# Optimization experiments

Hardware: AMD Instinct MI355X
Metric: run time of the kernel (lower is better)

The kernel has to match this reference:

```python
import jax, jax.numpy as jnp
import numpy as np

EMBED_DIM = 1024
NUM_HEADS = 16
HEAD_DIM = EMBED_DIM // NUM_HEADS
EPS = 1e-5


def setup_inputs() -> dict:
    key = jax.random.key(0)
    ks = jax.random.split(key, 7)
    B, S, D = 4, 2048, EMBED_DIM
    s = 1.0 / np.sqrt(D)
    return {
        "x": jax.random.normal(ks[0], (B, S, D), dtype=jnp.float32),
        "W_qkv": jax.random.uniform(ks[1], (D, 3 * D), jnp.float32, -s, s),
        "b_qkv": jax.random.uniform(ks[2], (3 * D,), jnp.float32, -s, s),
        "W_out": jax.random.uniform(ks[3], (D, D), jnp.float32, -s, s),
        "b_out": jax.random.uniform(ks[4], (D,), jnp.float32, -s, s),
        "gamma": jnp.ones((D,), jnp.float32),
        "beta": jnp.zeros((D,), jnp.float32),
    }


def _layer_norm(y, gamma, beta):
    mu = jnp.mean(y, axis=-1, keepdims=True)
    var = jnp.mean(jnp.square(y - mu), axis=-1, keepdims=True)
    return (y - mu) * jax.lax.rsqrt(var + EPS) * gamma + beta


def reference(x, W_qkv, b_qkv, W_out, b_out, gamma, beta):
    B, S, D = x.shape
    H, Hd = NUM_HEADS, HEAD_DIM
    qkv = x @ W_qkv + b_qkv                       # [B,S,3D]
    q, k, v = jnp.split(qkv, 3, axis=-1)
    q = q.reshape(B, S, H, Hd).transpose(0, 2, 1, 3)  # [B,H,S,Hd]
    k = k.reshape(B, S, H, Hd).transpose(0, 2, 1, 3)
    v = v.reshape(B, S, H, Hd).transpose(0, 2, 1, 3)
    scale = 1.0 / np.sqrt(Hd)
    scores = jnp.einsum("bhsd,bhtd->bhst", q, k) * scale  # [B,H,S,S]
    attn = jax.nn.softmax(scores, axis=-1)
    ctx = jnp.einsum("bhst,bhtd->bhsd", attn, v)  # [B,H,S,Hd]
    ctx = ctx.transpose(0, 2, 1, 3).reshape(B, S, D)
    out = ctx @ W_out + b_out
    return _layer_norm(out + x, gamma, beta)
```

## Files before the change

### kernel.cpp

```cpp
#include <hip/hip_runtime.h>
#include <stdint.h>
#include <stddef.h>


#define SEQ    2048
#define DMODEL 1024
#define NHEAD  16
#define HDIM   64

typedef __attribute__((ext_vector_type(4))) float f32x4;
typedef __attribute__((ext_vector_type(16))) float f32x16;
typedef __attribute__((ext_vector_type(8))) short bf16x8;
typedef __attribute__((ext_vector_type(2))) unsigned uint2v;

static __device__ __forceinline__ unsigned short f2b(float f) {
  union { float f; unsigned u; } c; c.f = f;
  unsigned r = c.u + 0x7FFFu + ((c.u >> 16) & 1u);
  return (unsigned short)(r >> 16);
}
static __device__ __forceinline__ unsigned pkbf(float lo, float hi_) {
  unsigned r;
  asm("v_cvt_pk_bf16_f32 %0, %1, %2" : "=v"(r) : "v"(lo), "v"(hi_));
  return r;
}
static __device__ __forceinline__ float exp2v(float x) {
  return __builtin_amdgcn_exp2f(x);
}
static __device__ __forceinline__ uint2v swap32(unsigned a, unsigned b) {
  return __builtin_amdgcn_permlane32_swap(a, b, false, false);
}
static __device__ __forceinline__ void gl_lds16(const void* g, void* l) {
  __builtin_amdgcn_global_load_lds((const __attribute__((address_space(1))) void*)g,
                                   (__attribute__((address_space(3))) void*)l, 16, 0, 0);
}
static __device__ __forceinline__ int swz(int row, int col) {
  return (row * 64 + col) ^ ((row & 7) << 3);
}

__global__ __launch_bounds__(256) void k_cvt(const float* __restrict__ in,
                                             unsigned short* __restrict__ out) {
  const size_t i = ((size_t)blockIdx.x * 256 + threadIdx.x) * 8;
  f32x4 a = *(const f32x4*)&in[i];
  f32x4 b = *(const f32x4*)&in[i + 4];
  bf16x8 o;
  o[0] = (short)f2b(a[0]); o[1] = (short)f2b(a[1]);
  o[2] = (short)f2b(a[2]); o[3] = (short)f2b(a[3]);
  o[4] = (short)f2b(b[0]); o[5] = (short)f2b(b[1]);
  o[6] = (short)f2b(b[2]); o[7] = (short)f2b(b[3]);
  *(bf16x8*)&out[i] = o;
}

__global__ __launch_bounds__(256) void k_transpose_cvt(const float* __restrict__ in,
                                                       unsigned short* __restrict__ out,
                                                       int R, int C) {
  __shared__ unsigned short tile[32][33];
  const int c0 = blockIdx.x * 32, r0 = blockIdx.y * 32;
  const int tx = threadIdx.x, ty = threadIdx.y;
#pragma unroll
  for (int j = 0; j < 4; j++) {
    int rr = ty + j * 8;
    tile[rr][tx] = f2b(in[(size_t)(r0 + rr) * C + c0 + tx]);
  }
  __syncthreads();
#pragma unroll
  for (int j = 0; j < 4; j++) {
    int rr = ty + j * 8;
    out[(size_t)(c0 + rr) * R + r0 + tx] = tile[tx][rr];
  }
}

__global__ __launch_bounds__(256) void k_gemm_qkv(const unsigned short* __restrict__ X,
                                                  const unsigned short* __restrict__ WT,
                                                  const float* __restrict__ bias,
                                                  unsigned short* __restrict__ qb,
                                                  unsigned short* __restrict__ kb,
                                                  unsigned short* __restrict__ vt) {
  __shared__ __align__(16) unsigned short As[128 * 32];
  __shared__ __align__(16) unsigned short Bs[128 * 32];
  const int t = threadIdx.x;
  const int w = t >> 6, l = t & 63, g = l >> 4, r = l & 15;
  const int wr = w >> 1, wc = w & 1;
  const int bm = blockIdx.x * 128;
  const int bn = blockIdx.y * 128;

  f32x4 acc[4][4];
#pragma unroll
  for (int a = 0; a < 4; a++)
#pragma unroll
    for (int b = 0; b < 4; b++) acc[a][b] = f32x4{0.f, 0.f, 0.f, 0.f};

  for (int k0 = 0; k0 < DMODEL; k0 += 32) {
    __syncthreads();
#pragma unroll
    for (int j = 0; j < 2; j++) {
      int idx = t + j * 256;
      int row = idx >> 2, kc = idx & 3;
      gl_lds16(X + (size_t)(bm + row) * DMODEL + k0 + kc * 8, (char*)As + idx * 16);
      gl_lds16(WT + (size_t)(bn + row) * DMODEL + k0 + kc * 8, (char*)Bs + idx * 16);
    }
    __syncthreads();
    bf16x8 af[4], bf[4];
#pragma unroll
    for (int mf = 0; mf < 4; mf++)
      af[mf] = *(const bf16x8*)&As[(wr * 64 + mf * 16 + r) * 32 + g * 8];
#pragma unroll
    for (int nf = 0; nf < 4; nf++)
      bf[nf] = *(const bf16x8*)&Bs[(wc * 64 + nf * 16 + r) * 32 + g * 8];
#pragma unroll
    for (int mf = 0; mf < 4; mf++)
#pragma unroll
      for (int nf = 0; nf < 4; nf++)
        acc[mf][nf] = __builtin_amdgcn_mfma_f32_16x16x32_bf16(af[mf], bf[nf], acc[mf][nf], 0, 0, 0);
  }

#pragma unroll
  for (int mf = 0; mf < 4; mf++)
#pragma unroll
    for (int nf = 0; nf < 4; nf++)
#pragma unroll
      for (int i = 0; i < 4; i++) {
        int m = bm + wr * 64 + mf * 16 + g * 4 + i;
        int n = bn + wc * 64 + nf * 16 + r;
        float v = acc[mf][nf][i] + bias[n];
        int part = n >> 10, rem = n & 1023, h = rem >> 6, d = rem & 63;
        int bi = m >> 11, s = m & 2047;
        int bh = bi * NHEAD + h;
        if (part == 0)      qb[((size_t)bh * SEQ + s) * HDIM + d] = f2b(v * 0.18033688f);
        else if (part == 1) kb[((size_t)bh * SEQ + s) * HDIM + d] = f2b(v);
        else                vt[((size_t)bh * HDIM + d) * SEQ + s] = f2b(v);
      }
}

__global__ __launch_bounds__(256) void k_attn(const unsigned short* __restrict__ qb,
                                              const unsigned short* __restrict__ kb,
                                              const unsigned short* __restrict__ vt,
                                              unsigned short* __restrict__ ctx) {
  __shared__ __align__(16) unsigned short Qs[128 * 64];
  __shared__ __align__(16) unsigned short K0[64 * 64];
  __shared__ __align__(16) unsigned short V0[64 * 64];
  const int t = threadIdx.x;
  const int w = t >> 6, l = t & 63;
  const int ql = l & 31, hi = l >> 5;
  const int q0 = blockIdx.x * 128;
  const int bh = blockIdx.y;
  const size_t qoff = ((size_t)bh * SEQ + q0) * HDIM;

#pragma unroll
  for (int j = 0; j < 4; j++) {
    int idx = t + j * 256;
    int row = idx >> 3, s = idx & 7;
    gl_lds16(qb + qoff + (size_t)row * 64 + (s ^ (row & 7)) * 8, (char*)Qs + idx * 16);
  }
#pragma unroll
  for (int j = 0; j < 2; j++) {
    int idx = t + j * 256;
    int row = idx >> 3, s = idx & 7;
    gl_lds16(kb + ((size_t)bh * SEQ + row) * HDIM + (s ^ (row & 7)) * 8, (char*)K0 + idx * 16);
    gl_lds16(vt + ((size_t)bh * HDIM + row) * SEQ + (s ^ (row & 7)) * 8, (char*)V0 + idx * 16);
  }
  asm volatile("s_waitcnt vmcnt(4)" ::: "memory");
  __builtin_amdgcn_sched_barrier(0);
  __builtin_amdgcn_s_barrier();

  bf16x8 qf[4];
#pragma unroll
  for (int ds = 0; ds < 4; ds++)
    qf[ds] = *(const bf16x8*)&Qs[swz(w * 32 + ql, ds * 16 + hi * 8)];
  asm volatile("s_waitcnt lgkmcnt(0)" ::: "memory");
  __builtin_amdgcn_sched_barrier(0);
  __builtin_amdgcn_s_barrier();

  bf16x8 ones;
#pragma unroll
  for (int i = 0; i < 8; i++) ones[i] = (short)0x3F80;

  f32x16 acc_o[2];
  f32x16 acc_l;
#pragma unroll
  for (int db = 0; db < 2; db++)
#pragma unroll
    for (int i = 0; i < 16; i++) acc_o[db][i] = 0.f;
#pragma unroll
  for (int i = 0; i < 16; i++) acc_l[i] = 0.f;

  for (int it = 0; it < SEQ / 64; ++it) {
    const int b = it & 1;
    if (it + 1 < SEQ / 64) {
      const int kt = (it + 1) * 64;
      unsigned short* Kd = (b ^ 1) ? Qs : K0;
      unsigned short* Vd = (b ^ 1) ? (Qs + 4096) : V0;
#pragma unroll
      for (int j = 0; j < 2; j++) {
        int idx = t + j * 256;
        int row = idx >> 3, s = idx & 7;
        gl_lds16(kb + ((size_t)bh * SEQ + kt + row) * HDIM + (s ^ (row & 7)) * 8,
                 (char*)Kd + idx * 16);
        gl_lds16(vt + ((size_t)bh * HDIM + row) * SEQ + kt + (s ^ (row & 7)) * 8,
                 (char*)Vd + idx * 16);
      }
      asm volatile("s_waitcnt vmcnt(4)" ::: "memory");
    } else {
      asm volatile("s_waitcnt vmcnt(0)" ::: "memory");
    }
    __builtin_amdgcn_sched_barrier(0);
    __builtin_amdgcn_s_barrier();

    const unsigned short* Kb = b ? Qs : K0;
    const unsigned short* Vb = b ? (Qs + 4096) : V0;

    bf16x8 kf[2][4];
#pragma unroll
    for (int kb2 = 0; kb2 < 2; kb2++)
#pragma unroll
      for (int ds = 0; ds < 4; ds++)
        kf[kb2][ds] = *(const bf16x8*)&Kb[swz(kb2 * 32 + ql, ds * 16 + hi * 8)];

    f32x16 accs[2];
#pragma unroll
    for (int kb2 = 0; kb2 < 2; kb2++)
#pragma unroll
      for (int i = 0; i < 16; i++) accs[kb2][i] = 0.f;
    __builtin_amdgcn_s_setprio(1);
#pragma unroll
    for (int ds = 0; ds < 4; ds++)
#pragma unroll
      for (int kb2 = 0; kb2 < 2; kb2++)
        accs[kb2] = __builtin_amdgcn_mfma_f32_32x32x16_bf16(kf[kb2][ds], qf[ds], accs[kb2], 0, 0, 0);
    __builtin_amdgcn_s_setprio(0);

#pragma unroll
    for (int kb2 = 0; kb2 < 2; kb2++)
#pragma unroll
      for (int i = 0; i < 16; i++) accs[kb2][i] = exp2v(accs[kb2][i]);

    bf16x8 pa[4];
#pragma unroll
    for (int ks = 0; ks < 4; ks++) {
      const int kb2 = ks >> 1, rb = (ks & 1) * 8;
      unsigned wA0 = pkbf(accs[kb2][rb + 0], accs[kb2][rb + 1]);
      unsigned wA1 = pkbf(accs[kb2][rb + 2], accs[kb2][rb + 3]);
      unsigned wB0 = pkbf(accs[kb2][rb + 4], accs[kb2][rb + 5]);
      unsigned wB1 = pkbf(accs[kb2][rb + 6], accs[kb2][rb + 7]);
      uint2v s0 = swap32(wB0, wA0);
      uint2v s1 = swap32(wB1, wA1);
      union { bf16x8 v; unsigned u[4]; } fr;
      fr.u[0] = s0[1]; fr.u[1] = s1[1]; fr.u[2] = s0[0]; fr.u[3] = s1[0];
      pa[ks] = fr.v;
    }

    bf16x8 vf[2][4];
#pragma unroll
    for (int db = 0; db < 2; db++)
#pragma unroll
      for (int ks = 0; ks < 4; ks++)
        vf[db][ks] = *(const bf16x8*)&Vb[swz(db * 32 + ql, ks * 16 + hi * 8)];

    __builtin_amdgcn_s_setprio(1);
#pragma unroll
    for (int ks = 0; ks < 4; ks++) {
#pragma unroll
      for (int db = 0; db < 2; db++)
        acc_o[db] = __builtin_amdgcn_mfma_f32_32x32x16_bf16(vf[db][ks], pa[ks], acc_o[db], 0, 0, 0);
      acc_l = __builtin_amdgcn_mfma_f32_32x32x16_bf16(ones, pa[ks], acc_l, 0, 0, 0);
    }
    __builtin_amdgcn_s_setprio(0);

    __builtin_amdgcn_s_barrier();
  }

  const int bi = bh >> 4, h = bh & 15;
  const float rl = 1.f / acc_l[0];
  unsigned short* Ls = Qs + w * 2048;
#pragma unroll
  for (int db = 0; db < 2; db++)
#pragma unroll
    for (int j = 0; j < 8; j++) {
      const int d0 = db * 32 + (j & 1) * 2 + (j >> 1) * 8 + hi * 4;
      *(unsigned*)&Ls[(ql * 64 + d0) ^ ((ql & 7) << 3)] =
          pkbf(acc_o[db][2 * j] * rl, acc_o[db][2 * j + 1] * rl);
    }
#pragma unroll
  for (int rq = 0; rq < 4; rq++) {
    const int q = rq * 8 + (l >> 3);
    const int c8 = l & 7;
    bf16x8 ov = *(const bf16x8*)&Ls[(q * 64 + c8 * 8) ^ ((q & 7) << 3)];
    *(bf16x8*)&ctx[((size_t)bi * SEQ + q0 + w * 32 + q) * DMODEL + h * 64 + c8 * 8] = ov;
  }
}

__global__ __launch_bounds__(256) void k_gemm_out(const unsigned short* __restrict__ A,
                                                  const unsigned short* __restrict__ WT,
                                                  const float* __restrict__ bias,
                                                  const float* __restrict__ X,
                                                  float* __restrict__ Y) {
  __shared__ __align__(16) unsigned short As[128 * 32];
  __shared__ __align__(16) unsigned short Bs[128 * 32];
  const int t = threadIdx.x;
  const int w = t >> 6, l = t & 63, g = l >> 4, r = l & 15;
  const int wr = w >> 1, wc = w & 1;
  const int bm = blockIdx.x * 128;
  const int bn = blockIdx.y * 128;

  f32x4 acc[4][4];
#pragma unroll
  for (int a = 0; a < 4; a++)
#pragma unroll
    for (int b = 0; b < 4; b++) acc[a][b] = f32x4{0.f, 0.f, 0.f, 0.f};

  for (int k0 = 0; k0 < DMODEL; k0 += 32) {
    __syncthreads();
#pragma unroll
    for (int j = 0; j < 2; j++) {
      int idx = t + j * 256;
      int row = idx >> 2, kc = idx & 3;
      gl_lds16(A + (size_t)(bm + row) * DMODEL + k0 + kc * 8, (char*)As + idx * 16);
      gl_lds16(WT + (size_t)(bn + row) * DMODEL + k0 + kc * 8, (char*)Bs + idx * 16);
    }
    __syncthreads();
    bf16x8 af[4], bf[4];
#pragma unroll
    for (int mf = 0; mf < 4; mf++)
      af[mf] = *(const bf16x8*)&As[(wr * 64 + mf * 16 + r) * 32 + g * 8];
#pragma unroll
    for (int nf = 0; nf < 4; nf++)
      bf[nf] = *(const bf16x8*)&Bs[(wc * 64 + nf * 16 + r) * 32 + g * 8];
#pragma unroll
    for (int mf = 0; mf < 4; mf++)
#pragma unroll
      for (int nf = 0; nf < 4; nf++)
        acc[mf][nf] = __builtin_amdgcn_mfma_f32_16x16x32_bf16(af[mf], bf[nf], acc[mf][nf], 0, 0, 0);
  }

#pragma unroll
  for (int mf = 0; mf < 4; mf++)
#pragma unroll
    for (int nf = 0; nf < 4; nf++)
#pragma unroll
      for (int i = 0; i < 4; i++) {
        int m = bm + wr * 64 + mf * 16 + g * 4 + i;
        int n = bn + wc * 64 + nf * 16 + r;
        float v = acc[mf][nf][i] + bias[n] + X[(size_t)m * DMODEL + n];
        Y[(size_t)m * DMODEL + n] = v;
      }
}

__global__ __launch_bounds__(256) void k_ln(const float* __restrict__ Y,
                                            const float* __restrict__ gamma,
                                            const float* __restrict__ beta,
                                            float* __restrict__ out) {
  const int row = blockIdx.x, t = threadIdx.x;
  const float* y = Y + (size_t)row * DMODEL;
  f32x4 v = *(const f32x4*)&y[t * 4];
  float s = v[0] + v[1] + v[2] + v[3];
  float q = v[0] * v[0] + v[1] * v[1] + v[2] * v[2] + v[3] * v[3];
#pragma unroll
  for (int m = 1; m < 64; m <<= 1) { s += __shfl_xor(s, m); q += __shfl_xor(q, m); }
  __shared__ float ss[4], sq[4];
  const int w = t >> 6, l = t & 63;
  if (l == 0) { ss[w] = s; sq[w] = q; }
  __syncthreads();
  s = ss[0] + ss[1] + ss[2] + ss[3];
  q = sq[0] + sq[1] + sq[2] + sq[3];
  const float mu = s * (1.f / DMODEL);
  const float var = q * (1.f / DMODEL) - mu * mu;
  const float rs = rsqrtf(var + 1e-5f);
  f32x4 o;
#pragma unroll
  for (int j = 0; j < 4; j++)
    o[j] = (v[j] - mu) * rs * gamma[t * 4 + j] + beta[t * 4 + j];
  *(f32x4*)&out[(size_t)row * DMODEL + t * 4] = o;
}

extern "C" void kernel_launch(void* const* d_in, const int* in_sizes, int n_in,
                              void* d_out, int out_size, void* d_ws, size_t ws_size,
                              hipStream_t stream) {
  const float* X     = (const float*)d_in[0];
  const float* Wqkv  = (const float*)d_in[1];
  const float* bqkv  = (const float*)d_in[2];
  const float* Wout  = (const float*)d_in[3];
  const float* bout  = (const float*)d_in[4];
  const float* gamma = (const float*)d_in[5];
  const float* beta  = (const float*)d_in[6];

  char* ws = (char*)d_ws;
  unsigned short* wqkvT = (unsigned short*)(ws);
  unsigned short* woutT = (unsigned short*)(ws + 6291456);
  unsigned short* Xb    = (unsigned short*)(ws + 8388608);
  unsigned short* ctx   = (unsigned short*)(ws + 8388608);
  unsigned short* qb    = (unsigned short*)(ws + 25165824);
  unsigned short* kb    = (unsigned short*)(ws + 41943040);
  unsigned short* vt    = (unsigned short*)(ws + 58720256);
  float*          Yf    = (float*)d_out;

  dim3 tb(32, 8, 1);
  k_transpose_cvt<<<dim3(96, 32, 1), tb, 0, stream>>>(Wqkv, wqkvT, 1024, 3072);
  k_transpose_cvt<<<dim3(32, 32, 1), tb, 0, stream>>>(Wout, woutT, 1024, 1024);
  k_cvt<<<dim3(4096, 1, 1), dim3(256, 1, 1), 0, stream>>>(X, Xb);
  k_gemm_qkv<<<dim3(64, 24, 1), dim3(256, 1, 1), 0, stream>>>(Xb, wqkvT, bqkv, qb, kb, vt);
  k_attn<<<dim3(16, 64, 1), dim3(256, 1, 1), 0, stream>>>(qb, kb, vt, ctx);
  k_gemm_out<<<dim3(64, 8, 1), dim3(256, 1, 1), 0, stream>>>(ctx, woutT, bout, X, Yf);
  k_ln<<<dim3(8192, 1, 1), dim3(256, 1, 1), 0, stream>>>(Yf, gamma, beta, (float*)d_out);
}
```

Before: 232.7 us.

## Double-buffer LDS tiles and remap block IDs in QKV and output GEMMs

```diff
diff --git a/kernel.cpp b/kernel.cpp
--- a/kernel.cpp
+++ b/kernel.cpp
@@ -75,13 +75,15 @@
                                                   unsigned short* __restrict__ qb,
                                                   unsigned short* __restrict__ kb,
                                                   unsigned short* __restrict__ vt) {
-  __shared__ __align__(16) unsigned short As[128 * 32];
-  __shared__ __align__(16) unsigned short Bs[128 * 32];
+  __shared__ __align__(16) unsigned short As[2][128 * 32];
+  __shared__ __align__(16) unsigned short Bs[2][128 * 32];
   const int t = threadIdx.x;
   const int w = t >> 6, l = t & 63, g = l >> 4, r = l & 15;
   const int wr = w >> 1, wc = w & 1;
-  const int bm = blockIdx.x * 128;
-  const int bn = blockIdx.y * 128;
+  int id = blockIdx.x;
+  id = (id & 7) * 192 + (id >> 3);
+  const int bm = (id & 63) * 128;
+  const int bn = (id >> 6) * 128;
 
   f32x4 acc[4][4];
 #pragma unroll
@@ -89,28 +91,46 @@
 #pragma unroll
     for (int b = 0; b < 4; b++) acc[a][b] = f32x4{0.f, 0.f, 0.f, 0.f};
 
-  for (int k0 = 0; k0 < DMODEL; k0 += 32) {
-    __syncthreads();
-#pragma unroll
-    for (int j = 0; j < 2; j++) {
-      int idx = t + j * 256;
-      int row = idx >> 2, kc = idx & 3;
-      gl_lds16(X + (size_t)(bm + row) * DMODEL + k0 + kc * 8, (char*)As + idx * 16);
-      gl_lds16(WT + (size_t)(bn + row) * DMODEL + k0 + kc * 8, (char*)Bs + idx * 16);
-    }
-    __syncthreads();
+#pragma unroll
+  for (int j = 0; j < 2; j++) {
+    int idx = t + j * 256;
+    int row = idx >> 2, kc = idx & 3;
+    gl_lds16(X + (size_t)(bm + row) * DMODEL + kc * 8, (char*)As[0] + idx * 16);
+    gl_lds16(WT + (size_t)(bn + row) * DMODEL + kc * 8, (char*)Bs[0] + idx * 16);
+  }
+
+  for (int it = 0; it < DMODEL / 32; ++it) {
+    const int cur = it & 1;
+    if (it + 1 < DMODEL / 32) {
+      const int k0 = (it + 1) * 32;
+#pragma unroll
+      for (int j = 0; j < 2; j++) {
+        int idx = t + j * 256;
+        int row = idx >> 2, kc = idx & 3;
+        gl_lds16(X + (size_t)(bm + row) * DMODEL + k0 + kc * 8, (char*)As[cur ^ 1] + idx * 16);
+        gl_lds16(WT + (size_t)(bn + row) * DMODEL + k0 + kc * 8, (char*)Bs[cur ^ 1] + idx * 16);
+      }
+      asm volatile("s_waitcnt vmcnt(4)" ::: "memory");
+    } else {
+      asm volatile("s_waitcnt vmcnt(0)" ::: "memory");
+    }
+    __builtin_amdgcn_sched_barrier(0);
+    __builtin_amdgcn_s_barrier();
+
     bf16x8 af[4], bf[4];
 #pragma unroll
     for (int mf = 0; mf < 4; mf++)
-      af[mf] = *(const bf16x8*)&As[(wr * 64 + mf * 16 + r) * 32 + g * 8];
+      af[mf] = *(const bf16x8*)&As[cur][(wr * 64 + mf * 16 + r) * 32 + g * 8];
 #pragma unroll
     for (int nf = 0; nf < 4; nf++)
-      bf[nf] = *(const bf16x8*)&Bs[(wc * 64 + nf * 16 + r) * 32 + g * 8];
+      bf[nf] = *(const bf16x8*)&Bs[cur][(wc * 64 + nf * 16 + r) * 32 + g * 8];
 #pragma unroll
     for (int mf = 0; mf < 4; mf++)
 #pragma unroll
       for (int nf = 0; nf < 4; nf++)
         acc[mf][nf] = __builtin_amdgcn_mfma_f32_16x16x32_bf16(af[mf], bf[nf], acc[mf][nf], 0, 0, 0);
+
+    __builtin_amdgcn_s_barrier();
   }
 
 #pragma unroll
@@ -293,13 +313,15 @@
                                                   const float* __restrict__ bias,
                                                   const float* __restrict__ X,
                                                   float* __restrict__ Y) {
-  __shared__ __align__(16) unsigned short As[128 * 32];
-  __shared__ __align__(16) unsigned short Bs[128 * 32];
+  __shared__ __align__(16) unsigned short As[2][128 * 32];
+  __shared__ __align__(16) unsigned short Bs[2][128 * 32];
   const int t = threadIdx.x;
   const int w = t >> 6, l = t & 63, g = l >> 4, r = l & 15;
   const int wr = w >> 1, wc = w & 1;
-  const int bm = blockIdx.x * 128;
-  const int bn = blockIdx.y * 128;
+  int id = blockIdx.x;
+  id = (id & 7) * 64 + (id >> 3);
+  const int bm = (id & 63) * 128;
+  const int bn = (id >> 6) * 128;
 
   f32x4 acc[4][4];
 #pragma unroll
@@ -307,28 +329,46 @@
 #pragma unroll
     for (int b = 0; b < 4; b++) acc[a][b] = f32x4{0.f, 0.f, 0.f, 0.f};
 
-  for (int k0 = 0; k0 < DMODEL; k0 += 32) {
-    __syncthreads();
-#pragma unroll
-    for (int j = 0; j < 2; j++) {
-      int idx = t + j * 256;
-      int row = idx >> 2, kc = idx & 3;
-      gl_lds16(A + (size_t)(bm + row) * DMODEL + k0 + kc * 8, (char*)As + idx * 16);
-      gl_lds16(WT + (size_t)(bn + row) * DMODEL + k0 + kc * 8, (char*)Bs + idx * 16);
-    }
-    __syncthreads();
+#pragma unroll
+  for (int j = 0; j < 2; j++) {
+    int idx = t + j * 256;
+    int row = idx >> 2, kc = idx & 3;
+    gl_lds16(A + (size_t)(bm + row) * DMODEL + kc * 8, (char*)As[0] + idx * 16);
+    gl_lds16(WT + (size_t)(bn + row) * DMODEL + kc * 8, (char*)Bs[0] + idx * 16);
+  }
+
+  for (int it = 0; it < DMODEL / 32; ++it) {
+    const int cur = it & 1;
+    if (it + 1 < DMODEL / 32) {
+      const int k0 = (it + 1) * 32;
+#pragma unroll
+      for (int j = 0; j < 2; j++) {
+        int idx = t + j * 256;
+        int row = idx >> 2, kc = idx & 3;
+        gl_lds16(A + (size_t)(bm + row) * DMODEL + k0 + kc * 8, (char*)As[cur ^ 1] + idx * 16);
+        gl_lds16(WT + (size_t)(bn + row) * DMODEL + k0 + kc * 8, (char*)Bs[cur ^ 1] + idx * 16);
+      }
+      asm volatile("s_waitcnt vmcnt(4)" ::: "memory");
+    } else {
+      asm volatile("s_waitcnt vmcnt(0)" ::: "memory");
+    }
+    __builtin_amdgcn_sched_barrier(0);
+    __builtin_amdgcn_s_barrier();
+
     bf16x8 af[4], bf[4];
 #pragma unroll
     for (int mf = 0; mf < 4; mf++)
-      af[mf] = *(const bf16x8*)&As[(wr * 64 + mf * 16 + r) * 32 + g * 8];
+      af[mf] = *(const bf16x8*)&As[cur][(wr * 64 + mf * 16 + r) * 32 + g * 8];
 #pragma unroll
     for (int nf = 0; nf < 4; nf++)
-      bf[nf] = *(const bf16x8*)&Bs[(wc * 64 + nf * 16 + r) * 32 + g * 8];
+      bf[nf] = *(const bf16x8*)&Bs[cur][(wc * 64 + nf * 16 + r) * 32 + g * 8];
 #pragma unroll
     for (int mf = 0; mf < 4; mf++)
 #pragma unroll
       for (int nf = 0; nf < 4; nf++)
         acc[mf][nf] = __builtin_amdgcn_mfma_f32_16x16x32_bf16(af[mf], bf[nf], acc[mf][nf], 0, 0, 0);
+
+    __builtin_amdgcn_s_barrier();
   }
 
 #pragma unroll
@@ -396,8 +436,8 @@
   k_transpose_cvt<<<dim3(96, 32, 1), tb, 0, stream>>>(Wqkv, wqkvT, 1024, 3072);
   k_transpose_cvt<<<dim3(32, 32, 1), tb, 0, stream>>>(Wout, woutT, 1024, 1024);
   k_cvt<<<dim3(4096, 1, 1), dim3(256, 1, 1), 0, stream>>>(X, Xb);
-  k_gemm_qkv<<<dim3(64, 24, 1), dim3(256, 1, 1), 0, stream>>>(Xb, wqkvT, bqkv, qb, kb, vt);
+  k_gemm_qkv<<<dim3(1536, 1, 1), dim3(256, 1, 1), 0, stream>>>(Xb, wqkvT, bqkv, qb, kb, vt);
   k_attn<<<dim3(16, 64, 1), dim3(256, 1, 1), 0, stream>>>(qb, kb, vt, ctx);
-  k_gemm_out<<<dim3(64, 8, 1), dim3(256, 1, 1), 0, stream>>>(ctx, woutT, bout, X, Yf);
+  k_gemm_out<<<dim3(512, 1, 1), dim3(256, 1, 1), 0, stream>>>(ctx, woutT, bout, X, Yf);
   k_ln<<<dim3(8192, 1, 1), dim3(256, 1, 1), 0, stream>>>(Yf, gamma, beta, (float*)d_out);
 }
```

New measurement: 277.1 us. 1.19x slower.
